# Kernel optimization log

Measured on AMD Instinct MI355X. Metric: run time of the kernel, lower is better.

The kernel has to match this reference:

```python
import jax, jax.numpy as jnp
import numpy as np

N_NODES = 100000
K_HOPS = 10
ALPHA = 0.1


def gcn_conv(x, src, dst, W, b, num_nodes):
    # GCNConv: linear first (cheaper: out_dim small), then D^-1/2 (A+I) D^-1/2 aggregation
    h = x @ W  # [N, out]
    deg = jax.ops.segment_sum(jnp.ones_like(dst, dtype=h.dtype), dst, num_segments=num_nodes)
    dinv = jnp.where(deg > 0, jax.lax.rsqrt(deg), 0.0)
    norm = dinv[src] * dinv[dst]  # [E]
    msg = h[src] * norm[:, None]
    out = jax.ops.segment_sum(msg, dst, num_segments=num_nodes)
    return out + b


def _with_self_loops(edge_index, num_nodes):
    loops = jnp.arange(num_nodes, dtype=edge_index.dtype)
    src = jnp.concatenate([edge_index[0], loops])
    dst = jnp.concatenate([edge_index[1], loops])
    return src, dst


def setup_inputs() -> dict:
    key = jax.random.key(0)
    ks = jax.random.split(key, 8)
    n_feat, hidden, n_cls, n_edges = 512, 16, 7, 3200000
    x = jax.random.normal(ks[0], (N_NODES, n_feat), dtype=jnp.float32)
    edge_index = jax.random.randint(ks[1], (2, n_edges), 0, N_NODES, dtype=jnp.int64)
    W1 = jax.random.normal(ks[2], (n_feat, hidden), dtype=jnp.float32) * 0.05
    b1 = jnp.zeros((hidden,), dtype=jnp.float32)
    Wl = jax.random.normal(ks[3], (hidden, hidden), dtype=jnp.float32) * 0.25
    bl = jnp.zeros((hidden,), dtype=jnp.float32)
    W2 = jax.random.normal(ks[4], (hidden, n_cls), dtype=jnp.float32) * 0.25
    b2 = jnp.zeros((n_cls,), dtype=jnp.float32)
    return {"x": x, "edge_index": edge_index, "W1": W1, "b1": b1, "Wl": Wl, "bl": bl, "W2": W2, "b2": b2}


def reference(x, edge_index, W1, b1, Wl, bl, W2, b2):
    src, dst = _with_self_loops(edge_index, N_NODES)
    h = jax.nn.relu(gcn_conv(x, src, dst, W1, b1, N_NODES))
    def body(h, _):
        h = ALPHA * jax.nn.relu(h @ Wl + bl) + (1.0 - ALPHA) * h
        return h, None
    h, _ = jax.lax.scan(body, h, None, length=K_HOPS)
    out = gcn_conv(h, src, dst, W2, b2, N_NODES)
    return jax.nn.log_softmax(out, axis=1)
```

## Files before the change

### kernel.cpp

```cpp
#include <hip/hip_runtime.h>
#include <math.h>

#define N_NODES 100000
#define N_EDGES 3200000
#define F_IN    512
#define HID     16
#define NCLS    7
#define ALPHA   0.1f
#define K_HOPS  10

#define SHIFT   7
#define BWIDTH  128
#define NBUCK   ((N_NODES + BWIDTH - 1) / BWIDTH)
#define CHUNK   8192
#define A3_BLOCKS ((N_EDGES + CHUNK - 1) / CHUNK)

#define OFF_BCNT    0u
#define OFF_BSTART  1024u
#define OFF_BCUR    2048u
#define OFF_RP      3072u
#define OFF_DINV    103424u
#define OFF_COL     203776u
#define OFF_BINNED  3403776u
#define OFF_H0      3403776u
#define OFF_H1      5003776u
#define OFF_Z       6603776u

__global__ void k_bhist(const int* __restrict__ dst, int* __restrict__ bcnt) {
    __shared__ int h[NBUCK];
    int tid = threadIdx.x;
    for (int i = tid; i < NBUCK; i += 256) h[i] = 0;
    __syncthreads();
    for (int e = blockIdx.x * 256 + tid; e < N_EDGES; e += gridDim.x * 256)
        atomicAdd(&h[dst[e] >> SHIFT], 1);
    __syncthreads();
    for (int i = tid; i < NBUCK; i += 256) {
        int v = h[i];
        if (v) atomicAdd(&bcnt[i], v);
    }
}

__global__ void k_bscan(const int* __restrict__ bcnt, int* __restrict__ bstart,
                        int* __restrict__ bcur) {
    __shared__ int s[1024];
    int tid = threadIdx.x;
    int v = (tid < NBUCK) ? bcnt[tid] : 0;
    s[tid] = v;
    __syncthreads();
    for (int off = 1; off < 1024; off <<= 1) {
        int t = (tid >= off) ? s[tid - off] : 0;
        __syncthreads();
        s[tid] += t;
        __syncthreads();
    }
    if (tid < NBUCK) {
        int ex = s[tid] - v;
        bstart[tid] = ex;
        bcur[tid] = ex;
    }
    if (tid == 0) bstart[NBUCK] = N_EDGES;
}

__global__ void k_bin(const int* __restrict__ src, const int* __restrict__ dst,
                      int* __restrict__ bcur, unsigned int* __restrict__ binned) {
    __shared__ int ha[1024];
    __shared__ int hb[1024];
    __shared__ int gbase[NBUCK];
    __shared__ int lcur[NBUCK];
    int tid = threadIdx.x;
    int e0 = blockIdx.x * CHUNK;
    int e1 = e0 + CHUNK;
    if (e1 > N_EDGES) e1 = N_EDGES;
    for (int i = tid; i < 1024; i += 256) ha[i] = 0;
    __syncthreads();
    for (int e = e0 + tid; e < e1; e += 256)
        atomicAdd(&ha[dst[e] >> SHIFT], 1);
    __syncthreads();
    int* a = ha;
    int* b = hb;
    for (int off = 1; off < 1024; off <<= 1) {
        for (int s = tid; s < 1024; s += 256)
            b[s] = a[s] + ((s >= off) ? a[s - off] : 0);
        __syncthreads();
        int* t = a; a = b; b = t;
    }
    for (int s = tid; s < NBUCK; s += 256) {
        int c = a[s] - ((s > 0) ? a[s - 1] : 0);
        lcur[s] = 0;
        gbase[s] = c ? atomicAdd(&bcur[s], c) : 0;
    }
    __syncthreads();
    for (int e = e0 + tid; e < e1; e += 256) {
        int d = dst[e];
        int bk = d >> SHIFT;
        int idx = atomicAdd(&lcur[bk], 1);
        binned[gbase[bk] + idx] =
            ((unsigned int)(d & (BWIDTH - 1)) << 17) | (unsigned int)src[e];
    }
}

__global__ void k_csr(const unsigned int* __restrict__ binned, const int* __restrict__ bstart,
                      int* __restrict__ rp, float* __restrict__ dinv, int* __restrict__ col) {
    __shared__ int cnt[BWIDTH];
    __shared__ int s[BWIDTH];
    __shared__ int cur[BWIDTH];
    int tid = threadIdx.x;
    int b = blockIdx.x;
    int base = b << SHIFT;
    int e0 = bstart[b], e1 = bstart[b + 1];
    if (tid < BWIDTH) cnt[tid] = 0;
    __syncthreads();
    for (int e = e0 + tid; e < e1; e += 256)
        atomicAdd(&cnt[binned[e] >> 17], 1);
    __syncthreads();
    int v = 0;
    if (tid < BWIDTH) { v = cnt[tid]; s[tid] = v; }
    __syncthreads();
    for (int off = 1; off < BWIDTH; off <<= 1) {
        int t = 0;
        if (tid < BWIDTH && tid >= off) t = s[tid - off];
        __syncthreads();
        if (tid < BWIDTH) s[tid] += t;
        __syncthreads();
    }
    if (tid < BWIDTH) {
        int ex = s[tid] - v;
        cur[tid] = ex;
        int node = base + tid;
        if (node < N_NODES) {
            rp[node] = e0 + ex;
            dinv[node] = rsqrtf((float)(v + 1));
        }
    }
    if (b == 0 && tid == 0) rp[N_NODES] = N_EDGES;
    __syncthreads();
    for (int e = e0 + tid; e < e1; e += 256) {
        unsigned int w = binned[e];
        int ln = (int)(w >> 17);
        int p = atomicAdd(&cur[ln], 1);
        col[e0 + p] = (int)(w & 0x1FFFFu);
    }
}

#define XW_ROWS 64
__global__ void k_xw1(const float* __restrict__ x, const float* __restrict__ W,
                      const float* __restrict__ dinv, float* __restrict__ h0s) {
    __shared__ float red[4][XW_ROWS][HID + 1];
    int lane = threadIdx.x & 63;
    int sp   = threadIdx.x >> 6;
    int rowBase = blockIdx.x * XW_ROWS;
    int row = rowBase + lane;
    float acc[HID];
#pragma unroll
    for (int c = 0; c < HID; c++) acc[c] = 0.f;
    if (row < N_NODES) {
        const float4* x4 = (const float4*)(x + (size_t)row * F_IN + sp * (F_IN / 4));
        for (int k4 = 0; k4 < F_IN / 16; k4++) {
            float4 xv = x4[k4];
            int kb = sp * (F_IN / 4) + k4 * 4;
#pragma unroll
            for (int j = 0; j < 4; j++) {
                float xj = (j == 0) ? xv.x : (j == 1) ? xv.y : (j == 2) ? xv.z : xv.w;
#pragma unroll
                for (int c = 0; c < HID; c++)
                    acc[c] += xj * W[(kb + j) * HID + c];
            }
        }
    }
#pragma unroll
    for (int c = 0; c < HID; c++) red[sp][lane][c] = acc[c];
    __syncthreads();
#pragma unroll
    for (int p = 0; p < 4; p++) {
        int f = threadIdx.x + p * 256;
        int r = f >> 4, c = f & 15;
        int node = rowBase + r;
        if (node < N_NODES) {
            float v = red[0][r][c] + red[1][r][c] + red[2][r][c] + red[3][r][c];
            h0s[(size_t)node * HID + c] = dinv[node] * v;
        }
    }
}

__global__ void k_agg1(const float* __restrict__ h0s, const int* __restrict__ rp,
                       const int* __restrict__ col, const float* __restrict__ dinv,
                       const float* __restrict__ b1, float* __restrict__ h1) {
    int t = blockIdx.x * blockDim.x + threadIdx.x;
    int node = t >> 4;
    int c = t & 15;
    if (node >= N_NODES) return;
    float acc = h0s[(size_t)node * HID + c];
    int e0 = rp[node], e1 = rp[node + 1];
    int e = e0;
    for (; e + 1 < e1; e += 2) {
        int s0 = col[e], s1 = col[e + 1];
        float v0 = h0s[(size_t)s0 * HID + c];
        float v1 = h0s[(size_t)s1 * HID + c];
        acc += v0;
        acc += v1;
    }
    if (e < e1) acc += h0s[(size_t)col[e] * HID + c];
    float o = dinv[node] * acc + b1[c];
    h1[(size_t)node * HID + c] = fmaxf(o, 0.f);
}

__global__ void k_hops(const float* __restrict__ h1, const float* __restrict__ Wl,
                       const float* __restrict__ bl, const float* __restrict__ W2,
                       const float* __restrict__ dinv, float* __restrict__ zs) {
    int node = blockIdx.x * blockDim.x + threadIdx.x;
    if (node >= N_NODES) return;
    float h[HID];
    const float4* h4 = (const float4*)(h1 + (size_t)node * HID);
#pragma unroll
    for (int q = 0; q < HID / 4; q++) {
        float4 v = h4[q];
        h[q * 4 + 0] = v.x; h[q * 4 + 1] = v.y;
        h[q * 4 + 2] = v.z; h[q * 4 + 3] = v.w;
    }
    for (int it = 0; it < K_HOPS; it++) {
        float tm[HID];
#pragma unroll
        for (int c = 0; c < HID; c++) tm[c] = bl[c];
#pragma unroll
        for (int k = 0; k < HID; k++) {
            float hk = h[k];
#pragma unroll
            for (int c = 0; c < HID; c++) tm[c] += hk * Wl[k * HID + c];
        }
#pragma unroll
        for (int c = 0; c < HID; c++)
            h[c] = ALPHA * fmaxf(tm[c], 0.f) + (1.f - ALPHA) * h[c];
    }
    float dv = dinv[node];
    float zz[8];
#pragma unroll
    for (int c = 0; c < 8; c++) zz[c] = 0.f;
#pragma unroll
    for (int k = 0; k < HID; k++) {
        float hk = h[k];
#pragma unroll
        for (int c = 0; c < NCLS; c++) zz[c] += hk * W2[k * NCLS + c];
    }
    float4* z4 = (float4*)(zs + (size_t)node * 8);
    float4 v0, v1;
    v0.x = dv * zz[0]; v0.y = dv * zz[1]; v0.z = dv * zz[2]; v0.w = dv * zz[3];
    v1.x = dv * zz[4]; v1.y = dv * zz[5]; v1.z = dv * zz[6]; v1.w = 0.f;
    z4[0] = v0; z4[1] = v1;
}

__global__ void k_agg2(const float* __restrict__ zs, const int* __restrict__ rp,
                       const int* __restrict__ col, const float* __restrict__ dinv,
                       const float* __restrict__ b2, float* __restrict__ out) {
    int t = blockIdx.x * blockDim.x + threadIdx.x;
    int node = t >> 3;
    int c = t & 7;
    if (node >= N_NODES) return;
    float acc = zs[(size_t)node * 8 + c];
    int e0 = rp[node], e1 = rp[node + 1];
    int e = e0;
    for (; e + 1 < e1; e += 2) {
        int s0 = col[e], s1 = col[e + 1];
        float v0 = zs[(size_t)s0 * 8 + c];
        float v1 = zs[(size_t)s1 * 8 + c];
        acc += v0;
        acc += v1;
    }
    if (e < e1) acc += zs[(size_t)col[e] * 8 + c];
    float o = dinv[node] * acc + ((c < NCLS) ? b2[c] : 0.f);
    float val = (c < NCLS) ? o : -INFINITY;
    float m = val;
    m = fmaxf(m, __shfl_xor(m, 1));
    m = fmaxf(m, __shfl_xor(m, 2));
    m = fmaxf(m, __shfl_xor(m, 4));
    float ex = (c < NCLS) ? expf(o - m) : 0.f;
    float ss = ex;
    ss += __shfl_xor(ss, 1);
    ss += __shfl_xor(ss, 2);
    ss += __shfl_xor(ss, 4);
    if (c < NCLS) out[(size_t)node * NCLS + c] = o - m - logf(ss);
}

extern "C" void kernel_launch(void* const* d_in, const int* in_sizes, int n_in,
                              void* d_out, int out_size, void* d_ws, size_t ws_size,
                              hipStream_t stream) {
    const float* x  = (const float*)d_in[0];
    const int*   ei = (const int*)d_in[1];
    const float* W1 = (const float*)d_in[2];
    const float* b1 = (const float*)d_in[3];
    const float* Wl = (const float*)d_in[4];
    const float* bl = (const float*)d_in[5];
    const float* W2 = (const float*)d_in[6];
    const float* b2 = (const float*)d_in[7];
    float* out = (float*)d_out;

    int*   wsI = (int*)d_ws;
    float* wsF = (float*)d_ws;
    int*          bcnt   = wsI + OFF_BCNT;
    int*          bstart = wsI + OFF_BSTART;
    int*          bcur   = wsI + OFF_BCUR;
    int*          rp     = wsI + OFF_RP;
    float*        dinv   = wsF + OFF_DINV;
    int*          col    = wsI + OFF_COL;
    unsigned int* binned = (unsigned int*)(wsI + OFF_BINNED);
    float*        h0s    = wsF + OFF_H0;
    float*        h1     = wsF + OFF_H1;
    float*        zs     = wsF + OFF_Z;

    const int* src = ei;
    const int* dst = ei + N_EDGES;

    hipMemsetAsync(bcnt, 0, NBUCK * sizeof(int), stream);

    k_bhist<<<1024, 256, 0, stream>>>(dst, bcnt);
    k_bscan<<<1, 1024, 0, stream>>>(bcnt, bstart, bcur);
    k_bin<<<A3_BLOCKS, 256, 0, stream>>>(src, dst, bcur, binned);
    k_csr<<<NBUCK, 256, 0, stream>>>(binned, bstart, rp, dinv, col);
    k_xw1<<<(N_NODES + XW_ROWS - 1) / XW_ROWS, 256, 0, stream>>>(x, W1, dinv, h0s);
    k_agg1<<<(N_NODES * 16 + 255) / 256, 256, 0, stream>>>(h0s, rp, col, dinv, b1, h1);
    k_hops<<<(N_NODES + 255) / 256, 256, 0, stream>>>(h1, Wl, bl, W2, dinv, zs);
    k_agg2<<<(N_NODES * 8 + 255) / 256, 256, 0, stream>>>(zs, rp, col, dinv, b2, out);
}
```

Before: 643.6 us.

## Stage x tiles in shared memory for XW1 and widen aggregation to full wavefronts

The x@W1 kernel now loads 32-column tiles of x with coalesced float4 reads, transposes them into double-buffered shared memory, and has each thread compute 4 output columns for one row. This replaces the per-thread strided row reads and the cross-split reduction. Both aggregation kernels now give each node a full 64-lane wavefront, spreading edges across lane groups and combining partial sums with shuffles. This adds memory-level parallelism for the gathers, at the cost of more threads and some idle lanes on low-degree nodes.

Measured after the change: 609.7 us. 1.06x faster.

```diff
diff --git a/kernel.cpp b/kernel.cpp
--- a/kernel.cpp
+++ b/kernel.cpp
@@ -143,65 +143,85 @@
 }
 
 #define XW_ROWS 64
+#define XW_KT   32
+#define XW_S    65
+#define XW_NT   (F_IN / XW_KT)
 __global__ void k_xw1(const float* __restrict__ x, const float* __restrict__ W,
                       const float* __restrict__ dinv, float* __restrict__ h0s) {
-    __shared__ float red[4][XW_ROWS][HID + 1];
-    int lane = threadIdx.x & 63;
-    int sp   = threadIdx.x >> 6;
+    __shared__ float xT[2][XW_KT * XW_S];
+    int tid = threadIdx.x;
     int rowBase = blockIdx.x * XW_ROWS;
-    int row = rowBase + lane;
-    float acc[HID];
-#pragma unroll
-    for (int c = 0; c < HID; c++) acc[c] = 0.f;
-    if (row < N_NODES) {
-        const float4* x4 = (const float4*)(x + (size_t)row * F_IN + sp * (F_IN / 4));
-        for (int k4 = 0; k4 < F_IN / 16; k4++) {
-            float4 xv = x4[k4];
-            int kb = sp * (F_IN / 4) + k4 * 4;
-#pragma unroll
-            for (int j = 0; j < 4; j++) {
-                float xj = (j == 0) ? xv.x : (j == 1) ? xv.y : (j == 2) ? xv.z : xv.w;
-#pragma unroll
-                for (int c = 0; c < HID; c++)
-                    acc[c] += xj * W[(kb + j) * HID + c];
-            }
+
+    int rf0 = tid >> 3, kq = tid & 7;
+    int rf1 = rf0 + 32;
+    bool v0 = (rowBase + rf0) < N_NODES;
+    bool v1 = (rowBase + rf1) < N_NODES;
+    const float* xrow0 = x + (size_t)(rowBase + rf0) * F_IN;
+    const float* xrow1 = x + (size_t)(rowBase + rf1) * F_IN;
+
+    int r  = tid & 63;
+    int cg = __builtin_amdgcn_readfirstlane(tid >> 6);
+    const float4* W4 = (const float4*)W;
+
+    float4 zero4 = make_float4(0.f, 0.f, 0.f, 0.f);
+    float4 acc = zero4;
+    float4 ld0 = v0 ? ((const float4*)xrow0)[kq] : zero4;
+    float4 ld1 = v1 ? ((const float4*)xrow1)[kq] : zero4;
+
+    for (int kt = 0; kt < XW_NT; kt++) {
+        int buf = kt & 1;
+        float* xb = xT[buf];
+        int kb = kq * 4;
+        xb[(kb + 0) * XW_S + rf0] = ld0.x;
+        xb[(kb + 1) * XW_S + rf0] = ld0.y;
+        xb[(kb + 2) * XW_S + rf0] = ld0.z;
+        xb[(kb + 3) * XW_S + rf0] = ld0.w;
+        xb[(kb + 0) * XW_S + rf1] = ld1.x;
+        xb[(kb + 1) * XW_S + rf1] = ld1.y;
+        xb[(kb + 2) * XW_S + rf1] = ld1.z;
+        xb[(kb + 3) * XW_S + rf1] = ld1.w;
+        if (kt + 1 < XW_NT) {
+            const float4* p0 = (const float4*)(xrow0 + (kt + 1) * XW_KT);
+            const float4* p1 = (const float4*)(xrow1 + (kt + 1) * XW_KT);
+            ld0 = v0 ? p0[kq] : zero4;
+            ld1 = v1 ? p1[kq] : zero4;
         }
-    }
-#pragma unroll
-    for (int c = 0; c < HID; c++) red[sp][lane][c] = acc[c];
-    __syncthreads();
-#pragma unroll
-    for (int p = 0; p < 4; p++) {
-        int f = threadIdx.x + p * 256;
-        int r = f >> 4, c = f & 15;
-        int node = rowBase + r;
-        if (node < N_NODES) {
-            float v = red[0][r][c] + red[1][r][c] + red[2][r][c] + red[3][r][c];
-            h0s[(size_t)node * HID + c] = dinv[node] * v;
+        __syncthreads();
+        const float* xr = &xb[r];
+#pragma unroll
+        for (int k = 0; k < XW_KT; k++) {
+            float xv = xr[k * XW_S];
+            float4 w4 = W4[(kt * XW_KT + k) * 4 + cg];
+            acc.x += xv * w4.x;
+            acc.y += xv * w4.y;
+            acc.z += xv * w4.z;
+            acc.w += xv * w4.w;
         }
+    }
+    int node = rowBase + r;
+    if (node < N_NODES) {
+        float dv = dinv[node];
+        float4 o;
+        o.x = dv * acc.x; o.y = dv * acc.y; o.z = dv * acc.z; o.w = dv * acc.w;
+        ((float4*)h0s)[(size_t)node * 4 + cg] = o;
     }
 }
 
 __global__ void k_agg1(const float* __restrict__ h0s, const int* __restrict__ rp,
                        const int* __restrict__ col, const float* __restrict__ dinv,
                        const float* __restrict__ b1, float* __restrict__ h1) {
-    int t = blockIdx.x * blockDim.x + threadIdx.x;
-    int node = t >> 4;
-    int c = t & 15;
+    int node = (blockIdx.x * blockDim.x + threadIdx.x) >> 6;
     if (node >= N_NODES) return;
-    float acc = h0s[(size_t)node * HID + c];
+    int lane = threadIdx.x & 63;
+    int c = lane & 15, eo = lane >> 4;
     int e0 = rp[node], e1 = rp[node + 1];
-    int e = e0;
-    for (; e + 1 < e1; e += 2) {
-        int s0 = col[e], s1 = col[e + 1];
-        float v0 = h0s[(size_t)s0 * HID + c];
-        float v1 = h0s[(size_t)s1 * HID + c];
-        acc += v0;
-        acc += v1;
-    }
-    if (e < e1) acc += h0s[(size_t)col[e] * HID + c];
-    float o = dinv[node] * acc + b1[c];
-    h1[(size_t)node * HID + c] = fmaxf(o, 0.f);
+    float acc = 0.f;
+    for (int e = e0 + eo; e < e1; e += 4)
+        acc += h0s[(size_t)col[e] * HID + c];
+    acc += __shfl_xor(acc, 16);
+    acc += __shfl_xor(acc, 32);
+    float o = dinv[node] * (acc + h0s[(size_t)node * HID + c]) + b1[c];
+    if (eo == 0) h1[(size_t)node * HID + c] = fmaxf(o, 0.f);
 }
 
 __global__ void k_hops(const float* __restrict__ h1, const float* __restrict__ Wl,
@@ -251,22 +271,18 @@
 __global__ void k_agg2(const float* __restrict__ zs, const int* __restrict__ rp,
                        const int* __restrict__ col, const float* __restrict__ dinv,
                        const float* __restrict__ b2, float* __restrict__ out) {
-    int t = blockIdx.x * blockDim.x + threadIdx.x;
-    int node = t >> 3;
-    int c = t & 7;
+    int node = (blockIdx.x * blockDim.x + threadIdx.x) >> 6;
     if (node >= N_NODES) return;
-    float acc = zs[(size_t)node * 8 + c];
+    int lane = threadIdx.x & 63;
+    int c = lane & 7, eo = lane >> 3;
     int e0 = rp[node], e1 = rp[node + 1];
-    int e = e0;
-    for (; e + 1 < e1; e += 2) {
-        int s0 = col[e], s1 = col[e + 1];
-        float v0 = zs[(size_t)s0 * 8 + c];
-        float v1 = zs[(size_t)s1 * 8 + c];
-        acc += v0;
-        acc += v1;
-    }
-    if (e < e1) acc += zs[(size_t)col[e] * 8 + c];
-    float o = dinv[node] * acc + ((c < NCLS) ? b2[c] : 0.f);
+    float acc = 0.f;
+    for (int e = e0 + eo; e < e1; e += 8)
+        acc += zs[(size_t)col[e] * 8 + c];
+    acc += __shfl_xor(acc, 8);
+    acc += __shfl_xor(acc, 16);
+    acc += __shfl_xor(acc, 32);
+    float o = dinv[node] * (acc + zs[(size_t)node * 8 + c]) + ((c < NCLS) ? b2[c] : 0.f);
     float val = (c < NCLS) ? o : -INFINITY;
     float m = val;
     m = fmaxf(m, __shfl_xor(m, 1));
@@ -277,7 +293,7 @@
     ss += __shfl_xor(ss, 1);
     ss += __shfl_xor(ss, 2);
     ss += __shfl_xor(ss, 4);
-    if (c < NCLS) out[(size_t)node * NCLS + c] = o - m - logf(ss);
+    if (eo == 0 && c < NCLS) out[(size_t)node * NCLS + c] = o - m - logf(ss);
 }
 
 extern "C" void kernel_launch(void* const* d_in, const int* in_sizes, int n_in,
@@ -316,7 +332,7 @@
     k_bin<<<A3_BLOCKS, 256, 0, stream>>>(src, dst, bcur, binned);
     k_csr<<<NBUCK, 256, 0, stream>>>(binned, bstart, rp, dinv, col);
     k_xw1<<<(N_NODES + XW_ROWS - 1) / XW_ROWS, 256, 0, stream>>>(x, W1, dinv, h0s);
-    k_agg1<<<(N_NODES * 16 + 255) / 256, 256, 0, stream>>>(h0s, rp, col, dinv, b1, h1);
+    k_agg1<<<(N_NODES * 64 + 255) / 256, 256, 0, stream>>>(h0s, rp, col, dinv, b1, h1);
     k_hops<<<(N_NODES + 255) / 256, 256, 0, stream>>>(h1, Wl, bl, W2, dinv, zs);
-    k_agg2<<<(N_NODES * 8 + 255) / 256, 256, 0, stream>>>(zs, rp, col, dinv, b2, out);
-}
+    k_agg2<<<(N_NODES * 64 + 255) / 256, 256, 0, stream>>>(zs, rp, col, dinv, b2, out);
+}
```
